# Performance work log

Hardware: AMD Instinct MI355X
Metric: run time of the kernel (lower is better)

Reference implementation:

```python
import jax, jax.numpy as jnp
import numpy as np

B, Q, D, T, S = 64, 1024, 256, 64, 3  # batch, queries, hidden_dim, targets/image, max_steps


def _hat(w):
    # (...,3) -> (...,3,3)
    z = jnp.zeros_like(w[..., 0])
    wx, wy, wz = w[..., 0], w[..., 1], w[..., 2]
    return jnp.stack([
        jnp.stack([z, -wz, wy], -1),
        jnp.stack([wz, z, -wx], -1),
        jnp.stack([-wy, wx, z], -1),
    ], -2)


def _vee(W):
    return jnp.stack([W[..., 2, 1] - W[..., 1, 2],
                      W[..., 0, 2] - W[..., 2, 0],
                      W[..., 1, 0] - W[..., 0, 1]], -1) * 0.5


def exp_SO3(omega):
    # Rodrigues: (...,3) -> (...,3,3)
    theta = jnp.clip(jnp.linalg.norm(omega, axis=-1, keepdims=True), 1e-12, None)  # (...,1)
    K = _hat(omega / theta)
    K2 = K @ K
    I = jnp.eye(3, dtype=omega.dtype)
    st = jnp.sin(theta)[..., None]
    ct = jnp.cos(theta)[..., None]
    R = I + st * K + (1.0 - ct) * K2
    Ho = _hat(omega)
    R_small = I + Ho + 0.5 * (Ho @ Ho)
    small = (theta[..., 0] < 1e-5).astype(omega.dtype)[..., None, None]
    return R * (1.0 - small) + R_small * small


def log_SO3(R):
    # (...,3,3) -> (...,3)
    tr = jnp.clip(R[..., 0, 0] + R[..., 1, 1] + R[..., 2, 2], -1.0, 3.0)
    theta = jnp.arccos(jnp.clip((tr - 1.0) * 0.5, -1.0, 1.0))[..., None]  # (...,1)
    W = 0.5 * (R - jnp.swapaxes(R, -1, -2))
    v = _vee(W)
    w = v / jnp.clip(jnp.sin(theta), 1e-12, None) * theta
    small = (theta[..., 0] < 1e-5).astype(R.dtype)[..., None]
    return w * (1.0 - small) + v * small


def _mlp(x, w1, b1, w2, b2):
    # Linear -> ReLU -> Linear -> Sigmoid
    h = jax.nn.relu(x @ w1 + b1)
    return jax.nn.sigmoid(h @ w2 + b2)


def setup_inputs() -> dict:
    key = jax.random.key(0)
    ks = iter(jax.random.split(key, 32))

    def lin(fin, fout):
        bound = 1.0 / np.sqrt(fin)
        kw, kb = jax.random.split(next(ks))
        w = jax.random.uniform(kw, (fin, fout), jnp.float32, -bound, bound)
        b = jax.random.uniform(kb, (fout,), jnp.float32, -bound, bound)
        return w, b

    R_pred = exp_SO3(0.5 * jax.random.normal(next(ks), (B, Q, 3), jnp.float32))
    t_pred = jax.random.normal(next(ks), (B, Q, 3), jnp.float32)
    pred_boxes = jax.random.uniform(next(ks), (B, Q, 4), jnp.float32)
    query_features = jax.random.normal(next(ks), (B, Q, D), jnp.float32)
    tgt_R = exp_SO3(0.5 * jax.random.normal(next(ks), (B, T, 3), jnp.float32))
    tgt_t = jax.random.normal(next(ks), (B, T, 3), jnp.float32)
    tgt_boxes = jax.random.uniform(next(ks), (B, T, 4), jnp.float32)
    tgt_features = jax.random.normal(next(ks), (B, T, D), jnp.float32)

    sp_w1, sp_b1 = lin(D, D // 2); sp_w2, sp_b2 = lin(D // 2, S)
    rw_w1, rw_b1 = lin(D, D // 2); rw_w2, rw_b2 = lin(D // 2, 1)
    tw_w1, tw_b1 = lin(D, D // 2); tw_w2, tw_b2 = lin(D // 2, 1)
    mn_w1, mn_b1 = lin(2 * D, D);  mn_w2, mn_b2 = lin(D, 1)
    global_strength = jnp.float32(0.5)

    return dict(R_pred=R_pred, t_pred=t_pred, pred_boxes=pred_boxes,
                query_features=query_features, tgt_R=tgt_R, tgt_t=tgt_t,
                tgt_boxes=tgt_boxes, tgt_features=tgt_features,
                sp_w1=sp_w1, sp_b1=sp_b1, sp_w2=sp_w2, sp_b2=sp_b2,
                rw_w1=rw_w1, rw_b1=rw_b1, rw_w2=rw_w2, rw_b2=rw_b2,
                tw_w1=tw_w1, tw_b1=tw_b1, tw_w2=tw_w2, tw_b2=tw_b2,
                mn_w1=mn_w1, mn_b1=mn_b1, mn_w2=mn_w2, mn_b2=mn_b2,
                global_strength=global_strength)


def reference(R_pred, t_pred, pred_boxes, query_features, tgt_R, tgt_t,
              tgt_boxes, tgt_features, sp_w1, sp_b1, sp_w2, sp_b2,
              rw_w1, rw_b1, rw_w2, rw_b2, tw_w1, tw_b1, tw_w2, tw_b2,
              mn_w1, mn_b1, mn_w2, mn_b2, global_strength):
    # adaptive per-step scales: (B,S)
    step_scales = _mlp(query_features.mean(axis=1), sp_w1, sp_b1, sp_w2, sp_b2)
    step_scales = step_scales * jnp.clip(global_strength, 0.0, 1.0)
    rot_w = _mlp(query_features, rw_w1, rw_b1, rw_w2, rw_b2)    # (B,Q,1)
    trans_w = _mlp(query_features, tw_w1, tw_b1, tw_w2, tw_b2)  # (B,Q,1)

    # nearest-neighbor matching on box centers
    c_pred = pred_boxes[..., :2]               # (B,Q,2)
    cgt = tgt_boxes[..., :2]                   # (B,T,2)
    d = jnp.sum((c_pred[:, :, None, :] - cgt[:, None, :, :]) ** 2, -1)  # (B,Q,T)
    nn_idx = jnp.argmin(d, axis=-1)            # (B,Q)

    matched_feat = jnp.take_along_axis(tgt_features, nn_idx[..., None], axis=1)  # (B,Q,D)
    combined = jnp.concatenate([query_features, matched_feat], -1)               # (B,Q,2D)
    match_w = _mlp(combined, mn_w1, mn_b1, mn_w2, mn_b2)                          # (B,Q,1)

    Rmatch = jnp.take_along_axis(tgt_R, nn_idx[..., None, None], axis=1)  # (B,Q,3,3)
    tmatch = jnp.take_along_axis(tgt_t, nn_idx[..., None], axis=1)        # (B,Q,3)

    Rb, tb = R_pred, t_pred
    for s in range(S):
        scale = step_scales[:, s][:, None, None]                 # (B,1,1)
        w = log_SO3(jnp.swapaxes(Rb, -1, -2) @ Rmatch)           # (B,Q,3)
        adaptive_w = w * rot_w * match_w * scale
        Rb = Rb @ exp_SO3(adaptive_w)
        tb = tb + (tmatch - tb) * trans_w * match_w * scale
    return Rb, tb
```

## Files before the change

### kernel.cpp

```cpp
#include <hip/hip_runtime.h>

typedef __bf16 bf16;
typedef __bf16 bf16x8 __attribute__((ext_vector_type(8)));
typedef float  f32x4  __attribute__((ext_vector_type(4)));

#define QTOT 1024
#define DD   256

__global__ void k_pack(const float* __restrict__ wr, const float* __restrict__ wt,
                       const float* __restrict__ wm, bf16* __restrict__ pk) {
  int gid = blockIdx.x * 256 + threadIdx.x;
  const float* W; int N, nK, idx; bf16* dst;
  if (gid < 4096)      { W = wr; N = 128; nK = 8;  idx = gid;        dst = pk; }
  else if (gid < 8192) { W = wt; N = 128; nK = 8;  idx = gid - 4096; dst = pk + 32768; }
  else                 { W = wm; N = 256; nK = 16; idx = gid - 8192; dst = pk + 65536; }
  int tile = idx >> 6, lane = idx & 63;
  int ni = tile / nK, ki = tile % nK;
  int l15 = lane & 15, quad = lane >> 4;
  int n = ni * 16 + l15;
  int kbase = ki * 32 + quad * 8;
  bf16x8 v;
#pragma unroll
  for (int j = 0; j < 8; ++j) v[j] = (bf16)W[(size_t)(kbase + j) * N + n];
  *(bf16x8*)(dst + (size_t)idx * 8) = v;
}

__global__ void k_mean(const float* __restrict__ qf, float* __restrict__ wsMean) {
  __shared__ float sPart[8][256];
  int b = blockIdx.x >> 3;
  int chunk = blockIdx.x & 7;
  int tid = threadIdx.x;
  int rg = tid >> 5, c8 = tid & 31;
  float acc[8] = {0.f,0.f,0.f,0.f,0.f,0.f,0.f,0.f};
  const float* base = qf + ((size_t)b * QTOT + (size_t)chunk * 128) * DD + c8 * 8;
  for (int it = 0; it < 16; ++it) {
    f32x4 v0 = *(const f32x4*)(base + (size_t)(it * 8 + rg) * DD);
    f32x4 v1 = *(const f32x4*)(base + (size_t)(it * 8 + rg) * DD + 4);
#pragma unroll
    for (int j = 0; j < 4; ++j) { acc[j] += v0[j]; acc[4 + j] += v1[j]; }
  }
#pragma unroll
  for (int j = 0; j < 8; ++j) sPart[rg][c8 * 8 + j] = acc[j];
  __syncthreads();
  float s = 0.f;
#pragma unroll
  for (int g = 0; g < 8; ++g) s += sPart[g][tid];
  atomicAdd(&wsMean[b * 256 + tid], s);
}

__global__ void k_scales(const float* __restrict__ wsMean,
                         const float* __restrict__ w1, const float* __restrict__ b1,
                         const float* __restrict__ w2, const float* __restrict__ b2,
                         const float* __restrict__ gs, float* __restrict__ outS) {
  __shared__ float sMean[256];
  __shared__ float sHid[128];
  int b = blockIdx.x, tid = threadIdx.x;
  sMean[tid]       = wsMean[b * 256 + tid]       * (1.f / 1024.f);
  sMean[tid + 128] = wsMean[b * 256 + tid + 128] * (1.f / 1024.f);
  __syncthreads();
  float h = b1[tid];
  for (int d = 0; d < 256; ++d) h += sMean[d] * w1[d * 128 + tid];
  sHid[tid] = fmaxf(h, 0.f);
  __syncthreads();
  if (tid < 3) {
    float o = b2[tid];
    for (int k = 0; k < 128; ++k) o += sHid[k] * w2[k * 3 + tid];
    float g = fminf(fmaxf(gs[0], 0.f), 1.f);
    outS[b * 3 + tid] = g / (1.f + expf(-o));
  }
}

__launch_bounds__(256, 2)
__global__ void k_main(const float* __restrict__ R_pred, const float* __restrict__ t_pred,
                       const float* __restrict__ pred_boxes, const float* __restrict__ qf,
                       const float* __restrict__ tgt_R, const float* __restrict__ tgt_t,
                       const float* __restrict__ tgt_boxes, const float* __restrict__ tgt_f,
                       const float* __restrict__ rw_b1, const float* __restrict__ rw_w2, const float* __restrict__ rw_b2,
                       const float* __restrict__ tw_b1, const float* __restrict__ tw_w2, const float* __restrict__ tw_b2,
                       const float* __restrict__ mn_b1, const float* __restrict__ mn_w2, const float* __restrict__ mn_b2,
                       const bf16* __restrict__ pk, const float* __restrict__ scales,
                       float* __restrict__ out) {
  __shared__ __align__(16) bf16 sQ[64 * 264];
  __shared__ __align__(16) bf16 sT[64 * 264];
  __shared__ float sRedA[4][64];
  __shared__ float sRedB[4][64];
  __shared__ float sCT[128];
  __shared__ int   sNN[64];
  __shared__ float sRW[64], sTW[64];

  const int tid = threadIdx.x;
  const int b  = blockIdx.x >> 4;
  const int qb = (blockIdx.x & 15) << 6;

  {
    const float* srcQ = qf + ((size_t)(b * QTOT + qb)) * DD;
    const float* srcT = tgt_f + ((size_t)b * 64) * DD;
#pragma unroll
    for (int it = 0; it < 8; ++it) {
      int idx = tid + it * 256;
      int row = idx >> 5, c8 = idx & 31;
      f32x4 q0 = *(const f32x4*)(srcQ + (size_t)row * DD + c8 * 8);
      f32x4 q1 = *(const f32x4*)(srcQ + (size_t)row * DD + c8 * 8 + 4);
      f32x4 t0 = *(const f32x4*)(srcT + (size_t)row * DD + c8 * 8);
      f32x4 t1 = *(const f32x4*)(srcT + (size_t)row * DD + c8 * 8 + 4);
      bf16x8 qv, tv;
#pragma unroll
      for (int j = 0; j < 4; ++j) {
        qv[j] = (bf16)q0[j]; qv[4 + j] = (bf16)q1[j];
        tv[j] = (bf16)t0[j]; tv[4 + j] = (bf16)t1[j];
      }
      *(bf16x8*)(sQ + row * 264 + c8 * 8) = qv;
      *(bf16x8*)(sT + row * 264 + c8 * 8) = tv;
    }
  }
  if (tid < 64) {
    sCT[2 * tid]     = tgt_boxes[((size_t)b * 64 + tid) * 4 + 0];
    sCT[2 * tid + 1] = tgt_boxes[((size_t)b * 64 + tid) * 4 + 1];
  }
  __syncthreads();
  if (tid < 64) {
    float px = pred_boxes[((size_t)(b * QTOT + qb + tid)) * 4 + 0];
    float py = pred_boxes[((size_t)(b * QTOT + qb + tid)) * 4 + 1];
    float best = 3.4e38f; int bi = 0;
    for (int t = 0; t < 64; ++t) {
      float dx = px - sCT[2 * t], dy = py - sCT[2 * t + 1];
      float d = __fadd_rn(__fmul_rn(dx, dx), __fmul_rn(dy, dy));
      if (d < best) { best = d; bi = t; }
    }
    sNN[tid] = bi;
  }
  __syncthreads();

  const int lane = tid & 63, wv = tid >> 6;
  const int l15 = lane & 15, quad = lane >> 4;
  const int koff = quad * 8;
  const bf16x8* pRot   = (const bf16x8*)pk;
  const bf16x8* pTrans = (const bf16x8*)(pk + 32768);
  const bf16x8* pMatch = (const bf16x8*)(pk + 65536);

  f32x4 accR[4][2], accT[4][2];
#pragma unroll
  for (int mt = 0; mt < 4; ++mt)
#pragma unroll
    for (int nl = 0; nl < 2; ++nl) {
      accR[mt][nl] = f32x4{0.f, 0.f, 0.f, 0.f};
      accT[mt][nl] = f32x4{0.f, 0.f, 0.f, 0.f};
    }
#pragma unroll
  for (int ks = 0; ks < 8; ++ks) {
    bf16x8 A[4];
#pragma unroll
    for (int mt = 0; mt < 4; ++mt)
      A[mt] = *(const bf16x8*)(sQ + (mt * 16 + l15) * 264 + ks * 32 + koff);
#pragma unroll
    for (int nl = 0; nl < 2; ++nl) {
      bf16x8 Br = pRot[((size_t)((2 * wv + nl) * 8 + ks)) * 64 + lane];
      bf16x8 Bt = pTrans[((size_t)((2 * wv + nl) * 8 + ks)) * 64 + lane];
#pragma unroll
      for (int mt = 0; mt < 4; ++mt) {
        accR[mt][nl] = __builtin_amdgcn_mfma_f32_16x16x32_bf16(A[mt], Br, accR[mt][nl], 0, 0, 0);
        accT[mt][nl] = __builtin_amdgcn_mfma_f32_16x16x32_bf16(A[mt], Bt, accT[mt][nl], 0, 0, 0);
      }
    }
  }
  {
    float b1r[2], w2r[2], b1t[2], w2t[2];
#pragma unroll
    for (int nl = 0; nl < 2; ++nl) {
      int n = (2 * wv + nl) * 16 + l15;
      b1r[nl] = rw_b1[n]; w2r[nl] = rw_w2[n];
      b1t[nl] = tw_b1[n]; w2t[nl] = tw_w2[n];
    }
#pragma unroll
    for (int mt = 0; mt < 4; ++mt)
#pragma unroll
      for (int i = 0; i < 4; ++i) {
        float pr = 0.f, pt = 0.f;
#pragma unroll
        for (int nl = 0; nl < 2; ++nl) {
          pr += fmaxf(accR[mt][nl][i] + b1r[nl], 0.f) * w2r[nl];
          pt += fmaxf(accT[mt][nl][i] + b1t[nl], 0.f) * w2t[nl];
        }
        pr += __shfl_xor(pr, 1); pr += __shfl_xor(pr, 2); pr += __shfl_xor(pr, 4); pr += __shfl_xor(pr, 8);
        pt += __shfl_xor(pt, 1); pt += __shfl_xor(pt, 2); pt += __shfl_xor(pt, 4); pt += __shfl_xor(pt, 8);
        if (l15 == 0) {
          int q = mt * 16 + quad * 4 + i;
          sRedA[wv][q] = pr; sRedB[wv][q] = pt;
        }
      }
  }
  __syncthreads();
  if (tid < 64) {
    float vr = sRedA[0][tid] + sRedA[1][tid] + sRedA[2][tid] + sRedA[3][tid] + rw_b2[0];
    float vt = sRedB[0][tid] + sRedB[1][tid] + sRedB[2][tid] + sRedB[3][tid] + tw_b2[0];
    sRW[tid] = 1.f / (1.f + expf(-vr));
    sTW[tid] = 1.f / (1.f + expf(-vt));
  }
  __syncthreads();

  f32x4 accM[4][4];
#pragma unroll
  for (int mt = 0; mt < 4; ++mt)
#pragma unroll
    for (int nl = 0; nl < 4; ++nl) accM[mt][nl] = f32x4{0.f, 0.f, 0.f, 0.f};
  int grow[4];
#pragma unroll
  for (int mt = 0; mt < 4; ++mt) grow[mt] = sNN[mt * 16 + l15];
#pragma unroll
  for (int ks = 0; ks < 16; ++ks) {
    bf16x8 A[4];
#pragma unroll
    for (int mt = 0; mt < 4; ++mt) {
      if (ks < 8)
        A[mt] = *(const bf16x8*)(sQ + (mt * 16 + l15) * 264 + ks * 32 + koff);
      else
        A[mt] = *(const bf16x8*)(sT + grow[mt] * 264 + (ks - 8) * 32 + koff);
    }
#pragma unroll
    for (int nl = 0; nl < 4; ++nl) {
      bf16x8 Bm = pMatch[((size_t)((4 * wv + nl) * 16 + ks)) * 64 + lane];
#pragma unroll
      for (int mt = 0; mt < 4; ++mt)
        accM[mt][nl] = __builtin_amdgcn_mfma_f32_16x16x32_bf16(A[mt], Bm, accM[mt][nl], 0, 0, 0);
    }
  }
  {
    float b1m[4], w2m[4];
#pragma unroll
    for (int nl = 0; nl < 4; ++nl) {
      int n = (4 * wv + nl) * 16 + l15;
      b1m[nl] = mn_b1[n]; w2m[nl] = mn_w2[n];
    }
#pragma unroll
    for (int mt = 0; mt < 4; ++mt)
#pragma unroll
      for (int i = 0; i < 4; ++i) {
        float pm = 0.f;
#pragma unroll
        for (int nl = 0; nl < 4; ++nl) pm += fmaxf(accM[mt][nl][i] + b1m[nl], 0.f) * w2m[nl];
        pm += __shfl_xor(pm, 1); pm += __shfl_xor(pm, 2); pm += __shfl_xor(pm, 4); pm += __shfl_xor(pm, 8);
        if (l15 == 0) sRedA[wv][mt * 16 + quad * 4 + i] = pm;
      }
  }
  __syncthreads();

  if (tid < 64) {
    float vm = sRedA[0][tid] + sRedA[1][tid] + sRedA[2][tid] + sRedA[3][tid] + mn_b2[0];
    float mw = 1.f / (1.f + expf(-vm));
    float rw = sRW[tid], tw = sTW[tid];
    size_t gq = (size_t)(b * QTOT + qb + tid);
    float R[9], Rm[9], t[3], tm[3];
#pragma unroll
    for (int i = 0; i < 9; ++i) R[i] = R_pred[gq * 9 + i];
#pragma unroll
    for (int c = 0; c < 3; ++c) t[c] = t_pred[gq * 3 + c];
    size_t gt = (size_t)b * 64 + sNN[tid];
#pragma unroll
    for (int i = 0; i < 9; ++i) Rm[i] = tgt_R[gt * 9 + i];
#pragma unroll
    for (int c = 0; c < 3; ++c) tm[c] = tgt_t[gt * 3 + c];

    for (int s = 0; s < 3; ++s) {
      float sc = scales[b * 3 + s];
      float cr = rw * mw * sc, ctr = tw * mw * sc;
      float Ax[9];
#pragma unroll
      for (int i = 0; i < 3; ++i)
#pragma unroll
        for (int j = 0; j < 3; ++j)
          Ax[i * 3 + j] = R[0 + i] * Rm[0 + j] + R[3 + i] * Rm[3 + j] + R[6 + i] * Rm[6 + j];
      float tr = fminf(fmaxf(Ax[0] + Ax[4] + Ax[8], -1.f), 3.f);
      float cthe = fminf(fmaxf((tr - 1.f) * 0.5f, -1.f), 1.f);
      float th = acosf(cthe);
      float vx = 0.5f * (Ax[7] - Ax[5]);
      float vy = 0.5f * (Ax[2] - Ax[6]);
      float vz = 0.5f * (Ax[3] - Ax[1]);
      float f = (th < 1e-5f) ? 1.f : th / fmaxf(sinf(th), 1e-12f);
      float ax = vx * f * cr, ay = vy * f * cr, az = vz * f * cr;
      float th2 = ax * ax + ay * ay + az * az;
      float thn = sqrtf(th2);
      float E[9];
      if (thn < 1e-5f) {
        E[0] = 1.f + 0.5f * (ax * ax - th2); E[1] = -az + 0.5f * ax * ay;        E[2] =  ay + 0.5f * ax * az;
        E[3] =  az + 0.5f * ax * ay;         E[4] = 1.f + 0.5f * (ay * ay - th2); E[5] = -ax + 0.5f * ay * az;
        E[6] = -ay + 0.5f * ax * az;         E[7] =  ax + 0.5f * ay * az;         E[8] = 1.f + 0.5f * (az * az - th2);
      } else {
        float kx = ax / thn, ky = ay / thn, kz = az / thn;
        float st = sinf(thn), co = cosf(thn), c1 = 1.f - co;
        E[0] = co + c1 * kx * kx;      E[1] = c1 * kx * ky - st * kz; E[2] = c1 * kx * kz + st * ky;
        E[3] = c1 * kx * ky + st * kz; E[4] = co + c1 * ky * ky;      E[5] = c1 * ky * kz - st * kx;
        E[6] = c1 * kx * kz - st * ky; E[7] = c1 * ky * kz + st * kx; E[8] = co + c1 * kz * kz;
      }
      float Rn[9];
#pragma unroll
      for (int i = 0; i < 3; ++i)
#pragma unroll
        for (int j = 0; j < 3; ++j)
          Rn[i * 3 + j] = R[i * 3 + 0] * E[j] + R[i * 3 + 1] * E[3 + j] + R[i * 3 + 2] * E[6 + j];
#pragma unroll
      for (int i = 0; i < 9; ++i) R[i] = Rn[i];
#pragma unroll
      for (int c = 0; c < 3; ++c) t[c] += (tm[c] - t[c]) * ctr;
    }
#pragma unroll
    for (int i = 0; i < 9; ++i) out[gq * 9 + i] = R[i];
#pragma unroll
    for (int c = 0; c < 3; ++c) out[(size_t)589824 + gq * 3 + c] = t[c];
  }
}

extern "C" void kernel_launch(void* const* d_in, const int* in_sizes, int n_in,
                              void* d_out, int out_size, void* d_ws, size_t ws_size,
                              hipStream_t stream) {
  const float* R_pred     = (const float*)d_in[0];
  const float* t_pred     = (const float*)d_in[1];
  const float* pred_boxes = (const float*)d_in[2];
  const float* qf         = (const float*)d_in[3];
  const float* tgt_R      = (const float*)d_in[4];
  const float* tgt_t      = (const float*)d_in[5];
  const float* tgt_boxes  = (const float*)d_in[6];
  const float* tgt_f      = (const float*)d_in[7];
  const float* sp_w1 = (const float*)d_in[8];
  const float* sp_b1 = (const float*)d_in[9];
  const float* sp_w2 = (const float*)d_in[10];
  const float* sp_b2 = (const float*)d_in[11];
  const float* rw_w1 = (const float*)d_in[12];
  const float* rw_b1 = (const float*)d_in[13];
  const float* rw_w2 = (const float*)d_in[14];
  const float* rw_b2 = (const float*)d_in[15];
  const float* tw_w1 = (const float*)d_in[16];
  const float* tw_b1 = (const float*)d_in[17];
  const float* tw_w2 = (const float*)d_in[18];
  const float* tw_b2 = (const float*)d_in[19];
  const float* mn_w1 = (const float*)d_in[20];
  const float* mn_b1 = (const float*)d_in[21];
  const float* mn_w2 = (const float*)d_in[22];
  const float* mn_b2 = (const float*)d_in[23];
  const float* gs    = (const float*)d_in[24];

  float* wsScales = (float*)d_ws;
  float* wsMean   = (float*)((char*)d_ws + 1024);
  bf16*  pk       = (bf16*)((char*)d_ws + 1024 + 65536);
  float* out      = (float*)d_out;

  hipMemsetAsync(wsMean, 0, 64 * 256 * sizeof(float), stream);
  k_pack<<<96, 256, 0, stream>>>(rw_w1, tw_w1, mn_w1, pk);
  k_mean<<<512, 256, 0, stream>>>(qf, wsMean);
  k_scales<<<64, 128, 0, stream>>>(wsMean, sp_w1, sp_b1, sp_w2, sp_b2, gs, wsScales);
  k_main<<<1024, 256, 0, stream>>>(R_pred, t_pred, pred_boxes, qf, tgt_R, tgt_t, tgt_boxes, tgt_f,
                                   rw_b1, rw_w2, rw_b2, tw_b1, tw_w2, tw_b2, mn_b1, mn_w2, mn_b2,
                                   pk, wsScales, out);
}
```

Baseline: 222.3 us.

## Merge pack/mean kernels, drop target smem staging, parallelize NN search

Merges the weight-packing and query-mean kernels into one launch and replaces the atomic mean accumulation (and its memset) with two per-batch partial sums combined in k_scales. k_main no longer stages target features in shared memory; the matched rows are gathered from global memory and converted to bf16 inside the second MFMA loop. This roughly halves shared memory, so launch bounds are raised to four blocks per CU. The nearest-neighbour search is split across four threads per query with a shuffle reduction, and the rot/trans weight results are kept in registers instead of going through shared memory, which removes one barrier. The trade-offs are a less parallel mean reduction (224 blocks instead of 512) and uncoalesced global gathers in the match GEMM.

```diff
diff --git a/kernel.cpp b/kernel.cpp
--- a/kernel.cpp
+++ b/kernel.cpp
@@ -7,56 +7,58 @@
 #define QTOT 1024
 #define DD   256
 
-__global__ void k_pack(const float* __restrict__ wr, const float* __restrict__ wt,
-                       const float* __restrict__ wm, bf16* __restrict__ pk) {
-  int gid = blockIdx.x * 256 + threadIdx.x;
-  const float* W; int N, nK, idx; bf16* dst;
-  if (gid < 4096)      { W = wr; N = 128; nK = 8;  idx = gid;        dst = pk; }
-  else if (gid < 8192) { W = wt; N = 128; nK = 8;  idx = gid - 4096; dst = pk + 32768; }
-  else                 { W = wm; N = 256; nK = 16; idx = gid - 8192; dst = pk + 65536; }
-  int tile = idx >> 6, lane = idx & 63;
-  int ni = tile / nK, ki = tile % nK;
-  int l15 = lane & 15, quad = lane >> 4;
-  int n = ni * 16 + l15;
-  int kbase = ki * 32 + quad * 8;
-  bf16x8 v;
-#pragma unroll
-  for (int j = 0; j < 8; ++j) v[j] = (bf16)W[(size_t)(kbase + j) * N + n];
-  *(bf16x8*)(dst + (size_t)idx * 8) = v;
+__global__ void k_prep(const float* __restrict__ wr, const float* __restrict__ wt,
+                       const float* __restrict__ wm, const float* __restrict__ qf,
+                       bf16* __restrict__ pk, float* __restrict__ wsMean2) {
+  __shared__ float sPart[8][256];
+  int blk = blockIdx.x;
+  if (blk < 96) {
+    int gid = blk * 256 + threadIdx.x;
+    const float* W; int N, nK, idx; bf16* dst;
+    if (gid < 4096)      { W = wr; N = 128; nK = 8;  idx = gid;        dst = pk; }
+    else if (gid < 8192) { W = wt; N = 128; nK = 8;  idx = gid - 4096; dst = pk + 32768; }
+    else                 { W = wm; N = 256; nK = 16; idx = gid - 8192; dst = pk + 65536; }
+    int tile = idx >> 6, lane = idx & 63;
+    int ni = tile / nK, ki = tile % nK;
+    int l15 = lane & 15, quad = lane >> 4;
+    int n = ni * 16 + l15;
+    int kbase = ki * 32 + quad * 8;
+    bf16x8 v;
+#pragma unroll
+    for (int j = 0; j < 8; ++j) v[j] = (bf16)W[(size_t)(kbase + j) * N + n];
+    *(bf16x8*)(dst + (size_t)idx * 8) = v;
+  } else {
+    int mb = blk - 96;
+    int b = mb >> 1, chunk = mb & 1;
+    int tid = threadIdx.x;
+    int rg = tid >> 5, c8 = tid & 31;
+    float acc[8] = {0.f,0.f,0.f,0.f,0.f,0.f,0.f,0.f};
+    const float* base = qf + ((size_t)b * QTOT + (size_t)chunk * 512) * DD + c8 * 8;
+    for (int it = 0; it < 64; ++it) {
+      f32x4 v0 = *(const f32x4*)(base + (size_t)(it * 8 + rg) * DD);
+      f32x4 v1 = *(const f32x4*)(base + (size_t)(it * 8 + rg) * DD + 4);
+#pragma unroll
+      for (int j = 0; j < 4; ++j) { acc[j] += v0[j]; acc[4 + j] += v1[j]; }
+    }
+#pragma unroll
+    for (int j = 0; j < 8; ++j) sPart[rg][c8 * 8 + j] = acc[j];
+    __syncthreads();
+    float s = 0.f;
+#pragma unroll
+    for (int g = 0; g < 8; ++g) s += sPart[g][tid];
+    wsMean2[mb * 256 + tid] = s;
+  }
 }
 
-__global__ void k_mean(const float* __restrict__ qf, float* __restrict__ wsMean) {
-  __shared__ float sPart[8][256];
-  int b = blockIdx.x >> 3;
-  int chunk = blockIdx.x & 7;
-  int tid = threadIdx.x;
-  int rg = tid >> 5, c8 = tid & 31;
-  float acc[8] = {0.f,0.f,0.f,0.f,0.f,0.f,0.f,0.f};
-  const float* base = qf + ((size_t)b * QTOT + (size_t)chunk * 128) * DD + c8 * 8;
-  for (int it = 0; it < 16; ++it) {
-    f32x4 v0 = *(const f32x4*)(base + (size_t)(it * 8 + rg) * DD);
-    f32x4 v1 = *(const f32x4*)(base + (size_t)(it * 8 + rg) * DD + 4);
-#pragma unroll
-    for (int j = 0; j < 4; ++j) { acc[j] += v0[j]; acc[4 + j] += v1[j]; }
-  }
-#pragma unroll
-  for (int j = 0; j < 8; ++j) sPart[rg][c8 * 8 + j] = acc[j];
-  __syncthreads();
-  float s = 0.f;
-#pragma unroll
-  for (int g = 0; g < 8; ++g) s += sPart[g][tid];
-  atomicAdd(&wsMean[b * 256 + tid], s);
-}
-
-__global__ void k_scales(const float* __restrict__ wsMean,
+__global__ void k_scales(const float* __restrict__ wsMean2,
                          const float* __restrict__ w1, const float* __restrict__ b1,
                          const float* __restrict__ w2, const float* __restrict__ b2,
                          const float* __restrict__ gs, float* __restrict__ outS) {
   __shared__ float sMean[256];
   __shared__ float sHid[128];
   int b = blockIdx.x, tid = threadIdx.x;
-  sMean[tid]       = wsMean[b * 256 + tid]       * (1.f / 1024.f);
-  sMean[tid + 128] = wsMean[b * 256 + tid + 128] * (1.f / 1024.f);
+  sMean[tid]       = (wsMean2[(b * 2) * 256 + tid]       + wsMean2[(b * 2 + 1) * 256 + tid])       * (1.f / 1024.f);
+  sMean[tid + 128] = (wsMean2[(b * 2) * 256 + tid + 128] + wsMean2[(b * 2 + 1) * 256 + tid + 128]) * (1.f / 1024.f);
   __syncthreads();
   float h = b1[tid];
   for (int d = 0; d < 256; ++d) h += sMean[d] * w1[d * 128 + tid];
@@ -70,7 +72,7 @@
   }
 }
 
-__launch_bounds__(256, 2)
+__launch_bounds__(256, 4)
 __global__ void k_main(const float* __restrict__ R_pred, const float* __restrict__ t_pred,
                        const float* __restrict__ pred_boxes, const float* __restrict__ qf,
                        const float* __restrict__ tgt_R, const float* __restrict__ tgt_t,
@@ -81,12 +83,10 @@
                        const bf16* __restrict__ pk, const float* __restrict__ scales,
                        float* __restrict__ out) {
   __shared__ __align__(16) bf16 sQ[64 * 264];
-  __shared__ __align__(16) bf16 sT[64 * 264];
   __shared__ float sRedA[4][64];
   __shared__ float sRedB[4][64];
-  __shared__ float sCT[128];
+  __shared__ float sRedM[4][64];
   __shared__ int   sNN[64];
-  __shared__ float sRW[64], sTW[64];
 
   const int tid = threadIdx.x;
   const int b  = blockIdx.x >> 4;
@@ -94,40 +94,38 @@
 
   {
     const float* srcQ = qf + ((size_t)(b * QTOT + qb)) * DD;
-    const float* srcT = tgt_f + ((size_t)b * 64) * DD;
 #pragma unroll
     for (int it = 0; it < 8; ++it) {
       int idx = tid + it * 256;
       int row = idx >> 5, c8 = idx & 31;
       f32x4 q0 = *(const f32x4*)(srcQ + (size_t)row * DD + c8 * 8);
       f32x4 q1 = *(const f32x4*)(srcQ + (size_t)row * DD + c8 * 8 + 4);
-      f32x4 t0 = *(const f32x4*)(srcT + (size_t)row * DD + c8 * 8);
-      f32x4 t1 = *(const f32x4*)(srcT + (size_t)row * DD + c8 * 8 + 4);
-      bf16x8 qv, tv;
-#pragma unroll
-      for (int j = 0; j < 4; ++j) {
-        qv[j] = (bf16)q0[j]; qv[4 + j] = (bf16)q1[j];
-        tv[j] = (bf16)t0[j]; tv[4 + j] = (bf16)t1[j];
-      }
+      bf16x8 qv;
+#pragma unroll
+      for (int j = 0; j < 4; ++j) { qv[j] = (bf16)q0[j]; qv[4 + j] = (bf16)q1[j]; }
       *(bf16x8*)(sQ + row * 264 + c8 * 8) = qv;
-      *(bf16x8*)(sT + row * 264 + c8 * 8) = tv;
-    }
-  }
-  if (tid < 64) {
-    sCT[2 * tid]     = tgt_boxes[((size_t)b * 64 + tid) * 4 + 0];
-    sCT[2 * tid + 1] = tgt_boxes[((size_t)b * 64 + tid) * 4 + 1];
-  }
-  __syncthreads();
-  if (tid < 64) {
-    float px = pred_boxes[((size_t)(b * QTOT + qb + tid)) * 4 + 0];
-    float py = pred_boxes[((size_t)(b * QTOT + qb + tid)) * 4 + 1];
-    float best = 3.4e38f; int bi = 0;
-    for (int t = 0; t < 64; ++t) {
-      float dx = px - sCT[2 * t], dy = py - sCT[2 * t + 1];
+    }
+  }
+  {
+    int q = tid >> 2, ch = tid & 3;
+    size_t gq = (size_t)(b * QTOT + qb + q);
+    float px = pred_boxes[gq * 4 + 0];
+    float py = pred_boxes[gq * 4 + 1];
+    const float* tb = tgt_boxes + ((size_t)b * 64 + ch * 16) * 4;
+    float best = 3.4e38f; int bi = ch * 16;
+    for (int i = 0; i < 16; ++i) {
+      f32x4 bx = *(const f32x4*)(tb + (size_t)i * 4);
+      float dx = px - bx[0], dy = py - bx[1];
       float d = __fadd_rn(__fmul_rn(dx, dx), __fmul_rn(dy, dy));
-      if (d < best) { best = d; bi = t; }
-    }
-    sNN[tid] = bi;
+      if (d < best) { best = d; bi = ch * 16 + i; }
+    }
+#pragma unroll
+    for (int m = 1; m < 4; m <<= 1) {
+      float pv = __shfl_xor(best, m);
+      int   pi = __shfl_xor(bi, m);
+      if (pv < best || (pv == best && pi < bi)) { best = pv; bi = pi; }
+    }
+    if ((tid & 3) == 0) sNN[q] = bi;
   }
   __syncthreads();
 
@@ -190,13 +188,15 @@
       }
   }
   __syncthreads();
-  if (tid < 64) {
-    float vr = sRedA[0][tid] + sRedA[1][tid] + sRedA[2][tid] + sRedA[3][tid] + rw_b2[0];
-    float vt = sRedB[0][tid] + sRedB[1][tid] + sRedB[2][tid] + sRedB[3][tid] + tw_b2[0];
-    sRW[tid] = 1.f / (1.f + expf(-vr));
-    sTW[tid] = 1.f / (1.f + expf(-vt));
-  }
-  __syncthreads();
+
+  float rw, tw;
+  {
+    int q = wv * 16 + l15;
+    float vr = sRedA[0][q] + sRedA[1][q] + sRedA[2][q] + sRedA[3][q] + rw_b2[0];
+    float vt = sRedB[0][q] + sRedB[1][q] + sRedB[2][q] + sRedB[3][q] + tw_b2[0];
+    rw = 1.f / (1.f + expf(-vr));
+    tw = 1.f / (1.f + expf(-vt));
+  }
 
   f32x4 accM[4][4];
 #pragma unroll
@@ -207,18 +207,33 @@
 #pragma unroll
   for (int mt = 0; mt < 4; ++mt) grow[mt] = sNN[mt * 16 + l15];
 #pragma unroll
-  for (int ks = 0; ks < 16; ++ks) {
+  for (int ks = 0; ks < 8; ++ks) {
     bf16x8 A[4];
 #pragma unroll
-    for (int mt = 0; mt < 4; ++mt) {
-      if (ks < 8)
-        A[mt] = *(const bf16x8*)(sQ + (mt * 16 + l15) * 264 + ks * 32 + koff);
-      else
-        A[mt] = *(const bf16x8*)(sT + grow[mt] * 264 + (ks - 8) * 32 + koff);
-    }
+    for (int mt = 0; mt < 4; ++mt)
+      A[mt] = *(const bf16x8*)(sQ + (mt * 16 + l15) * 264 + ks * 32 + koff);
 #pragma unroll
     for (int nl = 0; nl < 4; ++nl) {
       bf16x8 Bm = pMatch[((size_t)((4 * wv + nl) * 16 + ks)) * 64 + lane];
+#pragma unroll
+      for (int mt = 0; mt < 4; ++mt)
+        accM[mt][nl] = __builtin_amdgcn_mfma_f32_16x16x32_bf16(A[mt], Bm, accM[mt][nl], 0, 0, 0);
+    }
+  }
+#pragma unroll
+  for (int ks = 0; ks < 8; ++ks) {
+    bf16x8 A[4];
+#pragma unroll
+    for (int mt = 0; mt < 4; ++mt) {
+      const float* src = tgt_f + ((size_t)(b * 64 + grow[mt])) * DD + ks * 32 + koff;
+      f32x4 a0 = *(const f32x4*)src;
+      f32x4 a1 = *(const f32x4*)(src + 4);
+#pragma unroll
+      for (int j = 0; j < 4; ++j) { A[mt][j] = (bf16)a0[j]; A[mt][4 + j] = (bf16)a1[j]; }
+    }
+#pragma unroll
+    for (int nl = 0; nl < 4; ++nl) {
+      bf16x8 Bm = pMatch[((size_t)((4 * wv + nl) * 16 + 8 + ks)) * 64 + lane];
 #pragma unroll
       for (int mt = 0; mt < 4; ++mt)
         accM[mt][nl] = __builtin_amdgcn_mfma_f32_16x16x32_bf16(A[mt], Bm, accM[mt][nl], 0, 0, 0);
@@ -239,22 +254,22 @@
 #pragma unroll
         for (int nl = 0; nl < 4; ++nl) pm += fmaxf(accM[mt][nl][i] + b1m[nl], 0.f) * w2m[nl];
         pm += __shfl_xor(pm, 1); pm += __shfl_xor(pm, 2); pm += __shfl_xor(pm, 4); pm += __shfl_xor(pm, 8);
-        if (l15 == 0) sRedA[wv][mt * 16 + quad * 4 + i] = pm;
+        if (l15 == 0) sRedM[wv][mt * 16 + quad * 4 + i] = pm;
       }
   }
   __syncthreads();
 
-  if (tid < 64) {
-    float vm = sRedA[0][tid] + sRedA[1][tid] + sRedA[2][tid] + sRedA[3][tid] + mn_b2[0];
+  if (quad == 0) {
+    int q = wv * 16 + l15;
+    float vm = sRedM[0][q] + sRedM[1][q] + sRedM[2][q] + sRedM[3][q] + mn_b2[0];
     float mw = 1.f / (1.f + expf(-vm));
-    float rw = sRW[tid], tw = sTW[tid];
-    size_t gq = (size_t)(b * QTOT + qb + tid);
+    size_t gq = (size_t)(b * QTOT + qb + q);
     float R[9], Rm[9], t[3], tm[3];
 #pragma unroll
     for (int i = 0; i < 9; ++i) R[i] = R_pred[gq * 9 + i];
 #pragma unroll
     for (int c = 0; c < 3; ++c) t[c] = t_pred[gq * 3 + c];
-    size_t gt = (size_t)b * 64 + sNN[tid];
+    size_t gt = (size_t)b * 64 + sNN[q];
 #pragma unroll
     for (int i = 0; i < 9; ++i) Rm[i] = tgt_R[gt * 9 + i];
 #pragma unroll
@@ -339,14 +354,12 @@
   const float* gs    = (const float*)d_in[24];
 
   float* wsScales = (float*)d_ws;
-  float* wsMean   = (float*)((char*)d_ws + 1024);
-  bf16*  pk       = (bf16*)((char*)d_ws + 1024 + 65536);
+  float* wsMean2  = (float*)((char*)d_ws + 1024);
+  bf16*  pk       = (bf16*)((char*)d_ws + 1024 + 131072);
   float* out      = (float*)d_out;
 
-  hipMemsetAsync(wsMean, 0, 64 * 256 * sizeof(float), stream);
-  k_pack<<<96, 256, 0, stream>>>(rw_w1, tw_w1, mn_w1, pk);
-  k_mean<<<512, 256, 0, stream>>>(qf, wsMean);
-  k_scales<<<64, 128, 0, stream>>>(wsMean, sp_w1, sp_b1, sp_w2, sp_b2, gs, wsScales);
+  k_prep<<<224, 256, 0, stream>>>(rw_w1, tw_w1, mn_w1, qf, pk, wsMean2);
+  k_scales<<<64, 128, 0, stream>>>(wsMean2, sp_w1, sp_b1, sp_w2, sp_b2, gs, wsScales);
   k_main<<<1024, 256, 0, stream>>>(R_pred, t_pred, pred_boxes, qf, tgt_R, tgt_t, tgt_boxes, tgt_f,
                                    rw_b1, rw_w2, rw_b2, tw_b1, tw_w2, tw_b2, mn_b1, mn_w2, mn_b2,
                                    pk, wsScales, out);
```

Measured after the change: 237.3 us. 1.07x slower.
